# Optimization experiments

Measured on AMD Instinct MI355X. Metric: run time of the kernel, lower is better.

The kernel has to match this reference:

```python
import jax, jax.numpy as jnp
import numpy as np

IN_CH = 512
NUM_HEADS = 8
DEPTH = IN_CH // NUM_HEADS
IN_FEAT = 37


def setup_inputs() -> dict:
    key = jax.random.key(0)
    ks = jax.random.split(key, 9)
    B, S = 4, 2048
    s_in = 1.0 / np.sqrt(IN_FEAT)
    s_ch = 1.0 / np.sqrt(IN_CH)
    return {
        "x": jax.random.normal(ks[0], (B, S, IN_FEAT), dtype=jnp.float32),
        "Wq": jax.random.uniform(ks[1], (IN_FEAT, IN_CH), jnp.float32, -s_in, s_in),
        "bq": jax.random.uniform(ks[2], (IN_CH,), jnp.float32, -s_in, s_in),
        "Wk": jax.random.uniform(ks[3], (IN_FEAT, IN_CH), jnp.float32, -s_in, s_in),
        "bk": jax.random.uniform(ks[4], (IN_CH,), jnp.float32, -s_in, s_in),
        "Wv": jax.random.uniform(ks[5], (IN_FEAT, IN_CH), jnp.float32, -s_in, s_in),
        "bv": jax.random.uniform(ks[6], (IN_CH,), jnp.float32, -s_in, s_in),
        "Wd": jax.random.uniform(ks[7], (IN_CH, IN_CH), jnp.float32, -s_ch, s_ch),
        "bd": jax.random.uniform(ks[8], (IN_CH,), jnp.float32, -s_ch, s_ch),
    }


def reference(x, Wq, bq, Wk, bk, Wv, bv, Wd, bd):
    B, S, _ = x.shape
    # projections: [B,S,in_ch] -> split into [B,S,H,D]
    q = (x @ Wq + bq).reshape(B, S, NUM_HEADS, DEPTH)
    k = (x @ Wk + bk).reshape(B, S, NUM_HEADS, DEPTH)
    v = (x @ Wv + bv).reshape(B, S, NUM_HEADS, DEPTH)
    scale = 1.0 / jnp.sqrt(jnp.float32(DEPTH))
    # scores: [B,H,Sq,Sk]
    logits = jnp.einsum("bqhd,bkhd->bhqk", q, k) * scale
    attn = jax.nn.softmax(logits, axis=-1)
    out = jnp.einsum("bhqk,bkhd->bqhd", attn, v).reshape(B, S, IN_CH)
    return out @ Wd + bd
```

## Files before the change

kernel.cpp:

```cpp
#include <hip/hip_runtime.h>
#include <hip/hip_bf16.h>
#include <stdint.h>

#define IN_FEAT 37
#define IN_CH 512
#define NUM_HEADS 8
#define DEPTH 64
#define BB 4
#define SS 2048
#define NROWS (BB * SS)

typedef unsigned short u16;
typedef __attribute__((ext_vector_type(8))) short bf16x8;
typedef __attribute__((ext_vector_type(4))) float f32x4;
typedef __attribute__((ext_vector_type(16))) float f32x16;
typedef __attribute__((ext_vector_type(4))) unsigned u32x4;

#define MFMA16(a, b, c) __builtin_amdgcn_mfma_f32_16x16x32_bf16(a, b, c, 0, 0, 0)
#define MFMA32(a, b, c) __builtin_amdgcn_mfma_f32_32x32x16_bf16(a, b, c, 0, 0, 0)

#define GLDS16(gsrc, ldst)                                                          \
    __builtin_amdgcn_global_load_lds(                                               \
        reinterpret_cast<const __attribute__((address_space(1))) void*>(            \
            reinterpret_cast<uintptr_t>(gsrc)),                                     \
        reinterpret_cast<__attribute__((address_space(3))) void*>(                  \
            reinterpret_cast<uintptr_t>(ldst)),                                     \
        16, 0, 0)

__device__ __forceinline__ u16 f2bf(float f) {
    union { float f; unsigned u; } v;
    v.f = f;
    unsigned r = v.u + 0x7fffu + ((v.u >> 16) & 1u);
    return (u16)(r >> 16);
}

__device__ __forceinline__ unsigned cvt_pk_bf16(float a, float b) {
    unsigned r;
    asm("v_cvt_pk_bf16_f32 %0, %1, %2" : "=v"(r) : "v"(a), "v"(b));
    return r;
}

#define XB_ELEMS (NROWS * 64)
#define WT_ELEMS (IN_CH * 64)
#define WD_ELEMS (IN_CH * IN_CH)
#define PACK_TOTAL (XB_ELEMS + 3 * WT_ELEMS + WD_ELEMS)

__global__ __launch_bounds__(256) void pack_all(
    const float* __restrict__ x,
    const float* __restrict__ Wq, const float* __restrict__ Wk,
    const float* __restrict__ Wv, const float* __restrict__ Wd,
    u16* __restrict__ xb, u16* __restrict__ WqT, u16* __restrict__ WkT,
    u16* __restrict__ WvT, u16* __restrict__ WdT)
{
    const float QSC = 0.125f * 1.44269504f;
    int idx = blockIdx.x * 256 + threadIdx.x;
    if (idx < XB_ELEMS) {
        int row = idx >> 6, col = idx & 63;
        xb[idx] = (col < IN_FEAT) ? f2bf(x[row * IN_FEAT + col]) : (u16)0;
    } else if (idx < XB_ELEMS + 3 * WT_ELEMS) {
        int j = idx - XB_ELEMS;
        int mat = j >> 15, rem = j & (WT_ELEMS - 1);
        int c = rem >> 6, i = rem & 63;
        float v = 0.f;
        if (i < IN_FEAT) {
            if (mat == 0)      v = Wq[i * IN_CH + c] * QSC;
            else if (mat == 1) v = Wk[i * IN_CH + c];
            else               v = Wv[i * IN_CH + c];
        }
        (mat == 0 ? WqT : mat == 1 ? WkT : WvT)[rem] = f2bf(v);
    } else if (idx < PACK_TOTAL) {
        int j = idx - (XB_ELEMS + 3 * WT_ELEMS);
        int r = j >> 9, c = j & 511;
        WdT[c * IN_CH + r] = f2bf(Wd[j]);
    }
}

__global__ __launch_bounds__(256) void proj_qk(
    const u16* __restrict__ xb, const u16* __restrict__ WqT,
    const u16* __restrict__ WkT, const float* __restrict__ bqp,
    const float* __restrict__ bkp, u16* __restrict__ qo, u16* __restrict__ ko)
{
    const float QSC = 0.125f * 1.44269504f;
    const int tid = threadIdx.x;
    const int w = tid >> 6, lane = tid & 63;
    const int g = lane >> 4, l15 = lane & 15;
    const int m0 = blockIdx.x * 64 + w * 16;
    const int n0 = blockIdx.y * 64;
    const f32x4 Z4 = {0.f, 0.f, 0.f, 0.f};

    f32x4 aq[4], ak[4];
#pragma unroll
    for (int nt = 0; nt < 4; ++nt) { aq[nt] = Z4; ak[nt] = Z4; }

#pragma unroll
    for (int k0 = 0; k0 < 64; k0 += 32) {
        bf16x8 a = *(const bf16x8*)&xb[(m0 + l15) * 64 + k0 + g * 8];
#pragma unroll
        for (int nt = 0; nt < 4; ++nt) {
            bf16x8 bq8 = *(const bf16x8*)&WqT[(n0 + nt * 16 + l15) * 64 + k0 + g * 8];
            bf16x8 bk8 = *(const bf16x8*)&WkT[(n0 + nt * 16 + l15) * 64 + k0 + g * 8];
            aq[nt] = MFMA16(a, bq8, aq[nt]);
            ak[nt] = MFMA16(a, bk8, ak[nt]);
        }
    }
#pragma unroll
    for (int nt = 0; nt < 4; ++nt) {
        const int n = n0 + nt * 16 + l15;
        const float bqv = bqp[n] * QSC, bkv = bkp[n];
        const int h = n >> 6, d = n & 63;
#pragma unroll
        for (int r = 0; r < 4; ++r) {
            const int m = m0 + g * 4 + r;
            const int b = m >> 11, s = m & 2047;
            const int bh = b * NUM_HEADS + h;
            qo[(bh * SS + s) * DEPTH + d] = f2bf(aq[nt][r] + bqv);
            ko[bh * (SS * 64) + (s >> 6) * 4096 + (s & 63) * 64 + (d ^ ((s & 7) << 3))] =
                f2bf(ak[nt][r] + bkv);
        }
    }
}

__global__ __launch_bounds__(256) void proj_vT(
    const u16* __restrict__ WvT, const u16* __restrict__ xb,
    const float* __restrict__ bvp, u16* __restrict__ vo)
{
    const int tid = threadIdx.x;
    const int w = tid >> 6, lane = tid & 63;
    const int g = lane >> 4, l15 = lane & 15;
    const int m0 = blockIdx.x * 64 + w * 16;
    const int n0 = blockIdx.y * 64;
    const f32x4 Z4 = {0.f, 0.f, 0.f, 0.f};

    f32x4 acc[4];
#pragma unroll
    for (int nt = 0; nt < 4; ++nt) acc[nt] = Z4;

#pragma unroll
    for (int k0 = 0; k0 < 64; k0 += 32) {
        bf16x8 a = *(const bf16x8*)&WvT[(m0 + l15) * 64 + k0 + g * 8];
#pragma unroll
        for (int nt = 0; nt < 4; ++nt) {
            bf16x8 b8 = *(const bf16x8*)&xb[(n0 + nt * 16 + l15) * 64 + k0 + g * 8];
            acc[nt] = MFMA16(a, b8, acc[nt]);
        }
    }
    float bvr[4];
#pragma unroll
    for (int r = 0; r < 4; ++r) bvr[r] = bvp[m0 + g * 4 + r];
#pragma unroll
    for (int nt = 0; nt < 4; ++nt) {
#pragma unroll
        for (int r = 0; r < 4; ++r) {
            const int c = m0 + g * 4 + r;
            const int rr = n0 + nt * 16 + l15;
            const int b = rr >> 11, s = rr & 2047;
            const int h = c >> 6, d = c & 63;
            const int bh = b * NUM_HEADS + h;
            vo[bh * (SS * 64) + (s >> 6) * 4096 + d * 64 + ((s & 63) ^ ((d & 7) << 3))] =
                f2bf(acc[nt][r] + bvr[r]);
        }
    }
}

__global__ __launch_bounds__(256) void attn_kernel(
    const u16* __restrict__ Qm, const u16* __restrict__ Km,
    const u16* __restrict__ Vm, u16* __restrict__ Om)
{
    __shared__ u16 SM[16384];
    const int tid = threadIdx.x;
    const int w = tid >> 6, lane = tid & 63;
    const int r31 = lane & 31, lh = lane >> 5;
    const int qgrp = w >> 1, kh = w & 1;

    const int lin = blockIdx.x + gridDim.x * blockIdx.y;
    const int xcd = lin & 7, t7 = lin >> 3;
    const int bx = t7 & 31, bh = xcd + 8 * (t7 >> 5);
    const int qbase = bx * 64 + qgrp * 32;

    const u16* ktg = Km + bh * (SS * 64);
    const u16* vtg = Vm + bh * (SS * 64);

    bf16x8 Qf[4];
#pragma unroll
    for (int c = 0; c < 4; ++c)
        Qf[c] = *(const bf16x8*)&Qm[(bh * SS + qbase + r31) * 64 + c * 16 + lh * 8];

    f32x16 O0, O1;
#pragma unroll
    for (int i = 0; i < 16; ++i) { O0[i] = 0.f; O1[i] = 0.f; }
    float lreg = 0.f;

    auto STAGE = [&](int b, int t) {
        const u16* ks = ktg + t * 4096 + tid * 8;
        const u16* vs = vtg + t * 4096 + tid * 8;
        GLDS16(ks,        &SM[b * 4096 + w * 512]);
        GLDS16(ks + 2048, &SM[b * 4096 + 2048 + w * 512]);
        GLDS16(vs,        &SM[8192 + b * 4096 + w * 512]);
        GLDS16(vs + 2048, &SM[8192 + b * 4096 + 2048 + w * 512]);
    };

    int cur = 0;
    STAGE(0, 0);
    __syncthreads();

    const int krow = kh * 32 + r31;
    const int ksw = (krow & 7) << 3;

    for (int t = 0; t < SS / 64; ++t) {
        if (t < SS / 64 - 1) STAGE(cur ^ 1, t + 1);
        const u16* Kb = &SM[cur * 4096];
        const u16* Vb = &SM[8192 + cur * 4096];

        f32x16 s;
#pragma unroll
        for (int i = 0; i < 16; ++i) s[i] = 0.f;
#pragma unroll
        for (int c = 0; c < 4; ++c) {
            bf16x8 Kf = *(const bf16x8*)&Kb[krow * 64 + ((c * 16 + lh * 8) ^ ksw)];
            s = MFMA32(Kf, Qf[c], s);
        }

        unsigned pk[8];
        float ps = 0.f;
#pragma unroll
        for (int j = 0; j < 8; ++j) {
            float a = exp2f(s[2 * j]);
            float b = exp2f(s[2 * j + 1]);
            ps += a + b;
            pk[j] = cvt_pk_bf16(a, b);
        }
        lreg += ps;

        asm("v_permlane32_swap_b32 %0, %1" : "+v"(pk[0]), "+v"(pk[2]));
        asm("v_permlane32_swap_b32 %0, %1" : "+v"(pk[1]), "+v"(pk[3]));
        asm("v_permlane32_swap_b32 %0, %1" : "+v"(pk[4]), "+v"(pk[6]));
        asm("v_permlane32_swap_b32 %0, %1" : "+v"(pk[5]), "+v"(pk[7]));

        union { u32x4 u; bf16x8 b; } f0, f1;
        f0.u = (u32x4){pk[0], pk[1], pk[2], pk[3]};
        f1.u = (u32x4){pk[4], pk[5], pk[6], pk[7]};

#pragma unroll
        for (int dt = 0; dt < 2; ++dt) {
            const int vrow = dt * 32 + r31;
            const int vsw = (vrow & 7) << 3;
            bf16x8 Vf0 = *(const bf16x8*)&Vb[vrow * 64 + ((kh * 32 + lh * 8) ^ vsw)];
            bf16x8 Vf1 = *(const bf16x8*)&Vb[vrow * 64 + ((kh * 32 + 16 + lh * 8) ^ vsw)];
            if (dt == 0) {
                O0 = MFMA32(f0.b, Vf0, O0);
                O0 = MFMA32(f1.b, Vf1, O0);
            } else {
                O1 = MFMA32(f0.b, Vf0, O1);
                O1 = MFMA32(f1.b, Vf1, O1);
            }
        }
        __syncthreads();
        cur ^= 1;
    }

    float lfull = lreg + __shfl_xor(lreg, 32, 64);
    float* sc = (float*)&SM[0];
    float* scp = sc + qgrp * 2112;
    if (kh == 1) {
#pragma unroll
        for (int i = 0; i < 16; ++i) scp[i * 64 + lane] = O0[i];
#pragma unroll
        for (int i = 0; i < 16; ++i) scp[(16 + i) * 64 + lane] = O1[i];
        scp[2048 + lane] = lfull;
    }
    __syncthreads();
    if (kh == 0) {
#pragma unroll
        for (int i = 0; i < 16; ++i) O0[i] += scp[i * 64 + lane];
#pragma unroll
        for (int i = 0; i < 16; ++i) O1[i] += scp[(16 + i) * 64 + lane];
        const float inv = 1.0f / (lfull + scp[2048 + lane]);
        const int b = bh >> 3, hh = bh & 7;
#pragma unroll
        for (int i = 0; i < 16; ++i) {
            const int qr = (i & 3) + 8 * (i >> 2) + 4 * lh;
            const float invq = __shfl(inv, qr, 64);
            const int srow = qbase + qr;
            u16* orow = &Om[((b * SS + srow) << 9) + hh * 64];
            orow[r31]      = f2bf(O0[i] * invq);
            orow[32 + r31] = f2bf(O1[i] * invq);
        }
    }
}

__global__ __launch_bounds__(256) void out_gemm(
    const u16* __restrict__ A, const u16* __restrict__ BT,
    const float* __restrict__ bd, float* __restrict__ out)
{
    const int tid = threadIdx.x;
    const int w = tid >> 6, lane = tid & 63;
    const int g = lane >> 4, l15 = lane & 15;
    const int m0 = blockIdx.x * 64 + w * 16;
    const int n0 = blockIdx.y * 64;
    const f32x4 Z4 = {0.f, 0.f, 0.f, 0.f};

    f32x4 acc[4];
#pragma unroll
    for (int nt = 0; nt < 4; ++nt) acc[nt] = Z4;

    for (int k0 = 0; k0 < IN_CH; k0 += 32) {
        bf16x8 a = *(const bf16x8*)&A[(m0 + l15) * IN_CH + k0 + g * 8];
#pragma unroll
        for (int nt = 0; nt < 4; ++nt) {
            bf16x8 b = *(const bf16x8*)&BT[(n0 + nt * 16 + l15) * IN_CH + k0 + g * 8];
            acc[nt] = MFMA16(a, b, acc[nt]);
        }
    }
#pragma unroll
    for (int nt = 0; nt < 4; ++nt)
#pragma unroll
        for (int r = 0; r < 4; ++r) {
            const int m = m0 + g * 4 + r;
            const int n = n0 + nt * 16 + l15;
            out[m * IN_CH + n] = acc[nt][r] + bd[n];
        }
}

extern "C" void kernel_launch(void* const* d_in, const int* in_sizes, int n_in,
                              void* d_out, int out_size, void* d_ws, size_t ws_size,
                              hipStream_t stream)
{
    const float* x  = (const float*)d_in[0];
    const float* Wq = (const float*)d_in[1];
    const float* bq = (const float*)d_in[2];
    const float* Wk = (const float*)d_in[3];
    const float* bk = (const float*)d_in[4];
    const float* Wv = (const float*)d_in[5];
    const float* bv = (const float*)d_in[6];
    const float* Wd = (const float*)d_in[7];
    const float* bd = (const float*)d_in[8];
    float* out = (float*)d_out;

    u16* ws  = (u16*)d_ws;
    u16* q   = ws;
    u16* k   = q + NROWS * IN_CH;
    u16* vT  = k + NROWS * IN_CH;
    u16* ao  = vT + NROWS * IN_CH;
    u16* WdT = ao + NROWS * IN_CH;
    u16* xb  = WdT + WD_ELEMS;
    u16* WqT = xb + XB_ELEMS;
    u16* WkT = WqT + WT_ELEMS;
    u16* WvT = WkT + WT_ELEMS;

    pack_all<<<dim3((PACK_TOTAL + 255) / 256), dim3(256), 0, stream>>>(
        x, Wq, Wk, Wv, Wd, xb, WqT, WkT, WvT, WdT);
    proj_qk<<<dim3(NROWS / 64, IN_CH / 64), dim3(256), 0, stream>>>(
        xb, WqT, WkT, bq, bk, q, k);
    proj_vT<<<dim3(IN_CH / 64, NROWS / 64), dim3(256), 0, stream>>>(
        WvT, xb, bv, vT);
    attn_kernel<<<dim3(SS / 64, BB * NUM_HEADS), dim3(256), 0, stream>>>(q, k, vT, ao);
    out_gemm<<<dim3(NROWS / 64, IN_CH / 64), dim3(256), 0, stream>>>(ao, WdT, bd, out);
}
```

Measured before the change: 135.6 us.

## Use per-wave K staging and direct V register loads in attention loop

The attention main loop is restructured so each wave stages only its own K half into a private LDS double buffer. V fragments are loaded straight from global memory into registers, two tiles ahead. Synchronisation uses explicit vmcnt/lgkmcnt waits instead of a block-wide __syncthreads every iteration, which removes the barrier stall and lets loads overlap the MFMA work. The cost is duplicated K and V global traffic across query-group waves, more registers held for V fragments, and fragile hand-counted waitcnt logic.

```diff
diff --git a/kernel.cpp b/kernel.cpp
--- a/kernel.cpp
+++ b/kernel.cpp
@@ -162,11 +162,13 @@
     }
 }
 
+#define NT (SS / 64)
+
 __global__ __launch_bounds__(256) void attn_kernel(
     const u16* __restrict__ Qm, const u16* __restrict__ Km,
     const u16* __restrict__ Vm, u16* __restrict__ Om)
 {
-    __shared__ u16 SM[16384];
+    __shared__ u16 KL[4][2][2048];
     const int tid = threadIdx.x;
     const int w = tid >> 6, lane = tid & 63;
     const int r31 = lane & 31, lh = lane >> 5;
@@ -177,7 +179,7 @@
     const int bx = t7 & 31, bh = xcd + 8 * (t7 >> 5);
     const int qbase = bx * 64 + qgrp * 32;
 
-    const u16* ktg = Km + bh * (SS * 64);
+    const u16* ktg = Km + bh * (SS * 64) + kh * 2048;
     const u16* vtg = Vm + bh * (SS * 64);
 
     bf16x8 Qf[4];
@@ -190,35 +192,40 @@
     for (int i = 0; i < 16; ++i) { O0[i] = 0.f; O1[i] = 0.f; }
     float lreg = 0.f;
 
-    auto STAGE = [&](int b, int t) {
-        const u16* ks = ktg + t * 4096 + tid * 8;
-        const u16* vs = vtg + t * 4096 + tid * 8;
-        GLDS16(ks,        &SM[b * 4096 + w * 512]);
-        GLDS16(ks + 2048, &SM[b * 4096 + 2048 + w * 512]);
-        GLDS16(vs,        &SM[8192 + b * 4096 + w * 512]);
-        GLDS16(vs + 2048, &SM[8192 + b * 4096 + 2048 + w * 512]);
+    auto STAGE_K = [&](int buf, int t) {
+        const u16* ks = ktg + t * 4096 + lane * 8;
+        u16* kd = &KL[w][buf][0];
+#pragma unroll
+        for (int i = 0; i < 4; ++i) GLDS16(ks + i * 512, kd + i * 512);
     };
-
-    int cur = 0;
-    STAGE(0, 0);
-    __syncthreads();
-
-    const int krow = kh * 32 + r31;
-    const int ksw = (krow & 7) << 3;
-
-    for (int t = 0; t < SS / 64; ++t) {
-        if (t < SS / 64 - 1) STAGE(cur ^ 1, t + 1);
-        const u16* Kb = &SM[cur * 4096];
-        const u16* Vb = &SM[8192 + cur * 4096];
+    auto VLOAD = [&](bf16x8 (&v)[4], int t) {
+        const u16* vt = vtg + t * 4096;
+#pragma unroll
+        for (int dt = 0; dt < 2; ++dt)
+#pragma unroll
+            for (int o = 0; o < 2; ++o) {
+                const int vrow = dt * 32 + r31;
+                v[dt * 2 + o] = *(const bf16x8*)
+                    &vt[vrow * 64 + ((kh * 32 + o * 16 + lh * 8) ^ ((vrow & 7) << 3))];
+            }
+    };
+
+    auto STEP = [&](int buf, bf16x8 (&v)[4], int t, int waitN, bool stage) {
+        if (waitN == 8) asm volatile("s_waitcnt vmcnt(8)" ::: "memory");
+        else            asm volatile("s_waitcnt vmcnt(0)" ::: "memory");
+        __builtin_amdgcn_sched_barrier(0);
+
+        const u16* kb = &KL[w][buf][0];
+        bf16x8 kf[4];
+#pragma unroll
+        for (int c = 0; c < 4; ++c)
+            kf[c] = *(const bf16x8*)&kb[r31 * 64 + ((c * 16 + lh * 8) ^ ((r31 & 7) << 3))];
 
         f32x16 s;
 #pragma unroll
         for (int i = 0; i < 16; ++i) s[i] = 0.f;
 #pragma unroll
-        for (int c = 0; c < 4; ++c) {
-            bf16x8 Kf = *(const bf16x8*)&Kb[krow * 64 + ((c * 16 + lh * 8) ^ ksw)];
-            s = MFMA32(Kf, Qf[c], s);
-        }
+        for (int c = 0; c < 4; ++c) s = MFMA32(kf[c], Qf[c], s);
 
         unsigned pk[8];
         float ps = 0.f;
@@ -240,26 +247,37 @@
         f0.u = (u32x4){pk[0], pk[1], pk[2], pk[3]};
         f1.u = (u32x4){pk[4], pk[5], pk[6], pk[7]};
 
-#pragma unroll
-        for (int dt = 0; dt < 2; ++dt) {
-            const int vrow = dt * 32 + r31;
-            const int vsw = (vrow & 7) << 3;
-            bf16x8 Vf0 = *(const bf16x8*)&Vb[vrow * 64 + ((kh * 32 + lh * 8) ^ vsw)];
-            bf16x8 Vf1 = *(const bf16x8*)&Vb[vrow * 64 + ((kh * 32 + 16 + lh * 8) ^ vsw)];
-            if (dt == 0) {
-                O0 = MFMA32(f0.b, Vf0, O0);
-                O0 = MFMA32(f1.b, Vf1, O0);
-            } else {
-                O1 = MFMA32(f0.b, Vf0, O1);
-                O1 = MFMA32(f1.b, Vf1, O1);
-            }
-        }
-        __syncthreads();
-        cur ^= 1;
-    }
-
+        if (stage) {
+            asm volatile("s_waitcnt lgkmcnt(0)" ::: "memory");
+            __builtin_amdgcn_sched_barrier(0);
+            STAGE_K(buf, t + 2);
+        }
+
+        O0 = MFMA32(f0.b, v[0], O0);
+        O0 = MFMA32(f1.b, v[1], O0);
+        O1 = MFMA32(f0.b, v[2], O1);
+        O1 = MFMA32(f1.b, v[3], O1);
+
+        if (stage) VLOAD(v, t + 2);
+    };
+
+    bf16x8 vA[4], vB[4];
+    STAGE_K(0, 0);
+    VLOAD(vA, 0);
+    STAGE_K(1, 1);
+    VLOAD(vB, 1);
+
+    for (int tt = 0; tt < NT - 2; tt += 2) {
+        STEP(0, vA, tt,     8, tt + 2 < NT);
+        STEP(1, vB, tt + 1, 8, tt + 3 < NT);
+    }
+    STEP(0, vA, NT - 2, 8, false);
+    STEP(1, vB, NT - 1, 0, false);
+
+    asm volatile("s_waitcnt vmcnt(0)" ::: "memory");
+    __syncthreads();
     float lfull = lreg + __shfl_xor(lreg, 32, 64);
-    float* sc = (float*)&SM[0];
+    float* sc = (float*)&KL[0][0][0];
     float* scp = sc + qgrp * 2112;
     if (kh == 1) {
 #pragma unroll
```

After: 136.5 us. About the same (+0.7%).
